# Performance work log

Measured on AMD Instinct MI355X. Metric: run time of the kernel, lower is better.

The kernel has to match this reference:

```python
import jax, jax.numpy as jnp
import numpy as np

ALPHA, BETA, LAMB, GAMMA = 1.0, 1.0, 1e-4, 1.0
K_NN, TAU = 50, 0.1
EPS = 1e-8


def _sqdist(A, B):
    # ||a - b||^2, clamped at 0 like the torch code
    d2 = (A * A).sum(1)[:, None] + (B * B).sum(1)[None, :] - 2.0 * (A @ B.T)
    return jnp.maximum(d2, 0.0)


def _mmd(s, t):
    comb = jnp.concatenate([s, t], axis=0)
    sigma_sq = jax.lax.stop_gradient(jnp.median(_sqdist(comb, comb))) / 2.0
    sigma_sq = jnp.where(sigma_sq < 1e-6, jnp.float32(1.0), sigma_sq)
    g = 1.0 / (sigma_sq + EPS)
    kxx = jnp.exp(-g * _sqdist(s, s)).mean()
    kyy = jnp.exp(-g * _sqdist(t, t)).mean()
    kxy = jnp.exp(-g * _sqdist(s, t)).mean()
    return jnp.maximum(kxx + kyy - 2.0 * kxy, 0.0)


def setup_inputs() -> dict:
    key = jax.random.key(0)
    ks = jax.random.split(key, 8)
    B, d, N, Nq, K = 256, 128, 200000, 10000, K_NN
    q_batch = jax.random.normal(ks[0], (B, d), jnp.float32)
    X = jax.random.normal(ks[1], (N, d), jnp.float32)
    W = jax.random.normal(ks[2], (d, d), jnp.float32) * (1.0 / np.sqrt(d))
    b = jnp.zeros((d,), jnp.float32)
    pre_weights = jax.random.uniform(ks[3], (Nq, K), jnp.float32)
    pre_weights = pre_weights / pre_weights.sum(1, keepdims=True)
    pre_indices = jax.random.randint(ks[4], (Nq, K), 0, N)
    q_indices = jax.random.randint(ks[5], (B,), 0, Nq)
    idx = jax.random.randint(ks[6], (B,), 0, N)
    return {"q_batch": q_batch, "X": X, "W": W, "b": b,
            "pre_weights": pre_weights, "pre_indices": pre_indices,
            "q_indices": q_indices, "idx": idx}


def reference(q_batch, X, W, b, pre_weights, pre_indices, q_indices, idx):
    Tq = q_batch @ W.T + b                                   # model(q_batch), Linear(d, d)
    # ---- MMD between mapped queries and a random database batch ----
    loss_dist = _mmd(Tq, X[idx])
    # ---- exact KNN (faiss IndexFlatL2 equivalent) on detached embeddings ----
    d2_all = _sqdist(jax.lax.stop_gradient(Tq), X)           # [B, N]
    _, post_idx = jax.lax.top_k(-d2_all, K_NN)               # [B, K] nearest neighbors
    Xn = X[post_idx]                                         # [B, K, d]
    l2 = ((Tq[:, None, :] - Xn) ** 2).sum(-1)                # [B, K] (grad flows here)
    post_w = jax.nn.softmax(-l2 / TAU, axis=1)
    # ---- union-KL, vectorized over batch (exact torch.unique semantics) ----
    pre_i = pre_indices[q_indices]                           # [B, K]
    pre_w = pre_weights[q_indices]                           # [B, K]
    cat = jnp.concatenate([pre_i, post_idx], axis=1)         # [B, 2K]
    # multiplicity of each id within the concatenated list -> collapse duplicates
    mult = (cat[:, :, None] == cat[:, None, :]).sum(-1).astype(jnp.float32)  # [B, 2K]
    p_raw = jnp.einsum('bmk,bk->bm',
                       (cat[:, :, None] == pre_i[:, None, :]).astype(jnp.float32), pre_w)
    q_raw = jnp.einsum('bmk,bk->bm',
                       (cat[:, :, None] == post_idx[:, None, :]).astype(jnp.float32), post_w)
    p_c = jnp.maximum(p_raw, EPS)
    q_c = jnp.maximum(q_raw, EPS)
    p = p_c / (p_c / mult).sum(1, keepdims=True)             # normalize over union
    q = q_c / (q_c / mult).sum(1, keepdims=True)
    kl = ((p * (jnp.log(p) - jnp.log(q))) / mult).sum(1)     # KL(p || q) per sample
    loss_knn = kl.mean()
    # ---- L2 regularization of model params & anchor loss ----
    loss_reg = 0.5 * ((W ** 2).sum() + (b ** 2).sum())
    loss_anchor = ((Tq - q_batch) ** 2).sum(1).mean()
    total = ALPHA * loss_dist + BETA * loss_knn + LAMB * loss_reg + GAMMA * loss_anchor
    return jnp.stack([total, loss_dist, loss_knn, loss_anchor])
```

## Files before the change

kernel.cpp:

```cpp
#include <hip/hip_runtime.h>
#include <cstdint>

#define D 128
#define NPTS 200000
#define KNN 50
#define CAP 8192
#define NS 8192
#define SLACK 2.0f
#define EB 2048

#define OFF_ACC    0
#define OFF_SEL    256
#define OFF_CNT    1024
#define OFF_HIST0  17408
#define OFF_HIST12 148480
#define ZERO_BYTES 214016
#define OFF_COMB   214016
#define OFF_D2     476160
#define OFF_XN     1524736
#define OFF_SAMP   2324736
#define OFF_EBUF   2324736
#define OFF_THR    10713344
#define OFF_CANDI  10714368
#define OFF_BCNT   19102976
#define OFF_TQSW   27491584
#define OFF_XBF    27557120
#define OFF_ANCP   78757120
#define OFF_WREGP  78758144

typedef __attribute__((ext_vector_type(8))) short bf16x8;
typedef __attribute__((ext_vector_type(4))) float f32x4;
typedef const __attribute__((address_space(1))) void* gas_p;
typedef __attribute__((address_space(3))) void* las_p;

__device__ __forceinline__ unsigned fkey(float f) {
    unsigned u = __float_as_uint(f);
    return u ^ ((unsigned)((int)u >> 31) | 0x80000000u);
}

__device__ __forceinline__ void stage8k(const unsigned short* __restrict__ g,
                                        unsigned short* l, int w, int lane)
{
    #pragma unroll
    for (int j = 0; j < 2; j++) {
        const unsigned short* gp = g + j * 2048 + w * 512 + lane * 8;
        unsigned short* lp = l + j * 2048 + w * 512;
        __builtin_amdgcn_global_load_lds((gas_p)gp, (las_p)lp, 16, 0, 0);
    }
}

__global__ void k_phase1(const float* __restrict__ q, const float* __restrict__ X,
                         const float* __restrict__ W, const float* __restrict__ bb,
                         const int* __restrict__ idx, float* __restrict__ comb,
                         unsigned short* __restrict__ tqsw, unsigned short* __restrict__ xbf,
                         float* __restrict__ xn, float* __restrict__ ancp,
                         float* __restrict__ wregp, float* __restrict__ wszero)
{
    const int blk = blockIdx.x, t = threadIdx.x;
    if (blk < 12500) {
        __shared__ float xr4[4][16];
        const int lr = t & 15;
        const float4* src = (const float4*)(X + ((long)(blk * 16 + lr)) * D + (t >> 4) * 8);
        float4 v0 = src[0], v1 = src[1];
        uint4 pk;
        pk.x = (__float_as_uint(v0.x) >> 16) | (__float_as_uint(v0.y) & 0xFFFF0000u);
        pk.y = (__float_as_uint(v0.z) >> 16) | (__float_as_uint(v0.w) & 0xFFFF0000u);
        pk.z = (__float_as_uint(v1.x) >> 16) | (__float_as_uint(v1.y) & 0xFFFF0000u);
        pk.w = (__float_as_uint(v1.z) >> 16) | (__float_as_uint(v1.w) & 0xFFFF0000u);
        *(uint4*)(xbf + (long)blk * 2048 + t * 8) = pk;
        float ssq = v0.x*v0.x + v0.y*v0.y + v0.z*v0.z + v0.w*v0.w
                  + v1.x*v1.x + v1.y*v1.y + v1.z*v1.z + v1.w*v1.w;
        ssq += __shfl_down(ssq, 32);
        ssq += __shfl_down(ssq, 16);
        if ((t & 63) < 16) xr4[t >> 6][lr] = ssq;
        __syncthreads();
        if (t < 16) xn[blk * 16 + t] = xr4[0][t] + xr4[1][t] + xr4[2][t] + xr4[3][t];
    } else if (blk < 12628) {
        __shared__ float rowv[2][D];
        __shared__ float red[2][D];
        const int half = t >> 7, tt = t & 127;
        const int row = (blk - 12500) * 2 + half;
        rowv[half][tt] = q[row * D + tt];
        __syncthreads();
        float s = 0.f;
        const float* wr = W + tt * D;
        #pragma unroll 4
        for (int k = 0; k < D; k++) s = fmaf(rowv[half][k], wr[k], s);
        s += bb[tt];
        comb[row * D + tt] = s;
        unsigned ub = __float_as_uint(s);
        unsigned short hv = (unsigned short)((ub + 0x7fffu + ((ub >> 16) & 1u)) >> 16);
        int ksb = tt >> 5, quad = (tt & 31) >> 3, jj = tt & 7;
        int lane = quad * 16 + (row & 15);
        tqsw[(row >> 4) * 2048 + ksb * 512 + lane * 8 + jj] = hv;
        float dd = s - rowv[half][tt];
        red[half][tt] = dd * dd;
        __syncthreads();
        for (int off = 64; off > 0; off >>= 1) { if (tt < off) red[half][tt] += red[half][tt + off]; __syncthreads(); }
        if (tt == 0) ancp[row] = red[half][0];
    } else if (blk < 12756) {
        const int half = t >> 7, tt = t & 127;
        const int i = (blk - 12628) * 2 + half;
        comb[(256 + i) * D + tt] = X[(long)idx[i] * D + tt];
    } else if (blk < 12760) {
        __shared__ float wred[4];
        const int base = (blk - 12756) * 4096;
        float s = 0.f;
        #pragma unroll 4
        for (int k = 0; k < 16; k++) { float v = W[base + k * 256 + t]; s = fmaf(v, v, s); }
        if (blk == 12756 && t < D) { float v = bb[t]; s = fmaf(v, v, s); }
        #pragma unroll
        for (int off = 32; off > 0; off >>= 1) s += __shfl_down(s, off);
        if ((t & 63) == 0) wred[t >> 6] = s;
        __syncthreads();
        if (t == 0) wregp[blk - 12756] = wred[0] + wred[1] + wred[2] + wred[3];
    } else {
        uint4* z = (uint4*)wszero;
        const uint4 zz = make_uint4(0u, 0u, 0u, 0u);
        for (int i = (blk - 12760) * 256 + t; i < (ZERO_BYTES / 16); i += 1024) z[i] = zz;
    }
}

__global__ void k_d2m(const float* __restrict__ comb, float* __restrict__ D2w,
                      unsigned* __restrict__ hist0, const unsigned short* __restrict__ tqsw,
                      const unsigned short* __restrict__ xbf, const float* __restrict__ xn,
                      float* __restrict__ samp)
{
    __shared__ __align__(16) char smraw[51456];
    const int b = blockIdx.x, t = threadIdx.x;
    if (b < 1024) {
        float (*cj)[D + 1] = (float(*)[D + 1])smraw;
        float (*ci)[D]     = (float(*)[D])(smraw + 33024);
        unsigned* h        = (unsigned*)(smraw + 35072);
        const int ib = b >> 3, jb = b & 7;
        const int w = t >> 6, l = t & 63;
        for (int m = t; m < 4096; m += 256) h[m] = 0;
        const int irow = ib * 4 + w;
        ci[w][l] = comb[irow * D + l];
        ci[w][l + 64] = comb[irow * D + l + 64];
        const float4* src = (const float4*)(comb + (jb * 64) * D);
        #pragma unroll
        for (int m = 0; m < 8; m++) {
            int u = m * 256 + t;
            int r = u >> 5, c = u & 31;
            float4 v = src[u];
            cj[r][c * 4 + 0] = v.x; cj[r][c * 4 + 1] = v.y; cj[r][c * 4 + 2] = v.z; cj[r][c * 4 + 3] = v.w;
        }
        __syncthreads();
        float s = 0.f;
        #pragma unroll 4
        for (int k = 0; k < D; k++) { float d = ci[w][k] - cj[l][k]; s = fmaf(d, d, s); }
        D2w[irow * 512 + jb * 64 + l] = s;
        atomicAdd(&h[__float_as_uint(s) >> 20], 1u);
        __syncthreads();
        const int sh = (ib + jb) & 7;
        for (int m = t; m < 4096; m += 256) { unsigned v = h[m]; if (v) atomicAdd(&hist0[m * 8 + sh], v); }
    } else {
        unsigned short* sb = (unsigned short*)smraw;
        const int w = t >> 6, lane = t & 63;
        const int lr = lane & 15, quad = lane >> 4;
        const int ck = b - 1024;
        stage8k(xbf + (long)ck * 4096, sb, w, lane);
        bf16x8 a[4][4];
        #pragma unroll
        for (int i = 0; i < 4; i++)
            #pragma unroll
            for (int ks = 0; ks < 4; ks++)
                a[i][ks] = *(const bf16x8*)(tqsw + (w * 4 + i) * 2048 + ks * 512 + lane * 8);
        __syncthreads();
        #pragma unroll
        for (int tt = 0; tt < 2; tt++) {
            const int r = (ck * 2 + tt) * 16 + lr;
            float xnv = xn[r];
            bf16x8 bfr[4];
            #pragma unroll
            for (int ks = 0; ks < 4; ks++)
                bfr[ks] = *(const bf16x8*)(sb + tt * 2048 + ks * 512 + lane * 8);
            f32x4 acc4[4];
            #pragma unroll
            for (int i = 0; i < 4; i++) acc4[i] = (f32x4){0.f, 0.f, 0.f, 0.f};
            #pragma unroll
            for (int ks = 0; ks < 4; ks++)
                #pragma unroll
                for (int i = 0; i < 4; i++)
                    acc4[i] = __builtin_amdgcn_mfma_f32_16x16x32_bf16(a[i][ks], bfr[ks], acc4[i], 0, 0, 0);
            #pragma unroll
            for (int i = 0; i < 4; i++)
                #pragma unroll
                for (int reg = 0; reg < 4; reg++) {
                    int qq = w * 64 + i * 16 + quad * 4 + reg;
                    samp[qq * NS + r] = xnv - 2.f * acc4[i][reg];
                }
        }
    }
}

__global__ void k_h1thr(const float* __restrict__ D2w, unsigned* __restrict__ hist12,
                        const unsigned* __restrict__ hist0, unsigned* __restrict__ sel,
                        const float* __restrict__ samp, float* __restrict__ thr)
{
    __shared__ unsigned buf[8192];
    __shared__ unsigned bins[4096];
    __shared__ unsigned part[256];
    __shared__ unsigned selll[4];
    __shared__ unsigned wred[4];
    const int t = threadIdx.x;
    if (blockIdx.x < 256) {
        unsigned s = 0;
        #pragma unroll
        for (int m = 0; m < 16; m++) {
            int bin = t * 16 + m;
            unsigned bs = 0;
            #pragma unroll
            for (int sh = 0; sh < 8; sh++) bs += hist0[bin * 8 + sh];
            bins[bin] = bs;
            s += bs;
        }
        part[t] = s;
        for (int m = t; m < 8192; m += 256) buf[m] = 0;
        __syncthreads();
        if (t == 0) {
            for (int tg = 0; tg < 2; tg++) {
                unsigned r = tg ? 131072u : 131071u;
                int c = 0;
                while (part[c] <= r) { r -= part[c]; c++; }
                int b = c * 16;
                while (bins[b] <= r) { r -= bins[b]; b++; }
                selll[2 * tg] = (unsigned)b; selll[2 * tg + 1] = r;
            }
            if (blockIdx.x == 0) {
                sel[0] = selll[0]; sel[1] = selll[1]; sel[2] = selll[2]; sel[3] = selll[3];
            }
        }
        __syncthreads();
        unsigned p0 = selll[0], p1 = selll[2];
        const int e0 = blockIdx.x * 1024;
        for (int m = 0; m < 4; m++) {
            unsigned key = __float_as_uint(D2w[e0 + m * 256 + t]);
            if ((key >> 20) == p0) atomicAdd(&buf[(key >> 8) & 0xFFFu], 1u);
            if ((key >> 20) == p1) atomicAdd(&buf[4096 + ((key >> 8) & 0xFFFu)], 1u);
        }
        __syncthreads();
        for (int m = t; m < 8192; m += 256) { unsigned v = buf[m]; if (v) atomicAdd(&hist12[m], v); }
    } else {
        const int q = blockIdx.x - 256;
        unsigned kreg[32];
        #pragma unroll
        for (int i = 0; i < 32; i++) kreg[i] = fkey(samp[q * NS + i * 256 + t]);
        unsigned v = 0;
        for (int bit = 31; bit >= 0; bit--) {
            unsigned trial = v | (1u << bit);
            unsigned c = 0;
            #pragma unroll
            for (int i = 0; i < 32; i++) c += (kreg[i] < trial) ? 1u : 0u;
            #pragma unroll
            for (int off = 32; off > 0; off >>= 1) c += __shfl_down(c, off);
            if ((t & 63) == 0) wred[t >> 6] = c;
            __syncthreads();
            unsigned total = wred[0] + wred[1] + wred[2] + wred[3];
            __syncthreads();
            if (total <= (unsigned)(KNN - 1)) v = trial;
        }
        if (t == 0) {
            unsigned orig = (v & 0x80000000u) ? (v ^ 0x80000000u) : ~v;
            thr[q] = __uint_as_float(orig) + SLACK;
        }
    }
}

#define FILT_BODY(SBUF)                                                              \
    do {                                                                             \
        _Pragma("unroll")                                                            \
        for (int tt = 0; tt < 2; tt++) {                                             \
            const int r = (ck * 2 + tt) * 16 + lr;                                   \
            float xnv = xn[r];                                                       \
            bf16x8 bv[4];                                                            \
            _Pragma("unroll")                                                        \
            for (int ks2 = 0; ks2 < 4; ks2++)                                        \
                bv[ks2] = *(const bf16x8*)(SBUF + tt * 2048 + ks2 * 512 + lane * 8); \
            f32x4 acc4[4];                                                           \
            _Pragma("unroll")                                                        \
            for (int i = 0; i < 4; i++) acc4[i] = (f32x4){0.f, 0.f, 0.f, 0.f};       \
            _Pragma("unroll")                                                        \
            for (int ks2 = 0; ks2 < 4; ks2++)                                        \
                _Pragma("unroll")                                                    \
                for (int i = 0; i < 4; i++)                                          \
                    acc4[i] = __builtin_amdgcn_mfma_f32_16x16x32_bf16(a[i][ks2], bv[ks2], acc4[i], 0, 0, 0); \
            _Pragma("unroll")                                                        \
            for (int i = 0; i < 4; i++)                                              \
                _Pragma("unroll")                                                    \
                for (int reg = 0; reg < 4; reg++) {                                  \
                    float s = xnv - 2.f * acc4[i][reg];                              \
                    if (s <= th_r[i][reg]) {                                         \
                        unsigned qq = (unsigned)(w * 64 + i * 16 + quad * 4 + reg);  \
                        unsigned p = atomicAdd(&lcnt, 1u);                           \
                        if (p < 1024u) lbuf[p] = (qq << 18) | (unsigned)r;           \
                        else {                                                       \
                            unsigned dd2 = gbase + p;                                \
                            if (dd2 < EB) eb[dd2] = (qq << 18) | (unsigned)r;        \
                        }                                                            \
                    }                                                                \
                }                                                                    \
        }                                                                            \
    } while (0)

__global__ __launch_bounds__(256) void k_filt2(const unsigned short* __restrict__ tqsw,
    const unsigned short* __restrict__ xbf, const float* __restrict__ xn,
    const float* __restrict__ thr, unsigned* __restrict__ ebuf, unsigned* __restrict__ bcnt,
    const float* __restrict__ D2w, unsigned* __restrict__ hist12,
    unsigned* __restrict__ sel)
{
    if (blockIdx.x >= 1024) {
        __shared__ unsigned h2c[512];
        __shared__ unsigned part2[256];
        __shared__ unsigned pfx[2];
        __shared__ unsigned rr[2];
        const int t = threadIdx.x;
        for (int tg = 0; tg < 2; tg++) {
            const unsigned* hh = hist12 + tg * 4096;
            unsigned s = 0;
            for (int m = 0; m < 16; m++) s += hh[t * 16 + m];
            part2[t] = s;
            __syncthreads();
            if (t == 0) {
                unsigned r = sel[1 + 2 * tg];
                int c = 0;
                while (part2[c] <= r) { r -= part2[c]; c++; }
                int b = c * 16;
                while (hh[b] <= r) { r -= hh[b]; b++; }
                pfx[tg] = (sel[2 * tg] << 12) | (unsigned)b;
                rr[tg] = r;
            }
            __syncthreads();
        }
        if (blockIdx.x == 1024 && t == 0) {
            sel[4] = pfx[0]; sel[5] = rr[0]; sel[6] = pfx[1]; sel[7] = rr[1];
        }
        h2c[t] = 0; h2c[256 + t] = 0;
        __syncthreads();
        unsigned p0 = pfx[0], p1 = pfx[1];
        const int e0 = (blockIdx.x - 1024) * 1024;
        for (int m = 0; m < 4; m++) {
            unsigned key = __float_as_uint(D2w[e0 + m * 256 + t]);
            if ((key >> 8) == p0) atomicAdd(&h2c[key & 0xFFu], 1u);
            if ((key >> 8) == p1) atomicAdd(&h2c[256 + (key & 0xFFu)], 1u);
        }
        __syncthreads();
        unsigned* gp = hist12 + 8192;
        unsigned v0 = h2c[t], v1 = h2c[256 + t];
        if (v0) atomicAdd(&gp[t], v0);
        if (v1) atomicAdd(&gp[4096 + t], v1);
        return;
    }
    __shared__ unsigned short sbA[4096];
    __shared__ unsigned short sbB[4096];
    __shared__ unsigned lbuf[1024];
    __shared__ unsigned lcnt;
    __shared__ unsigned gbase;
    const int t = threadIdx.x;
    const int w = t >> 6, lane = t & 63;
    const int lr = lane & 15, quad = lane >> 4;
    unsigned* eb = ebuf + (unsigned)blockIdx.x * EB;
    bf16x8 a[4][4];
    #pragma unroll
    for (int i = 0; i < 4; i++)
        #pragma unroll
        for (int ks = 0; ks < 4; ks++)
            a[i][ks] = *(const bf16x8*)(tqsw + (w * 4 + i) * 2048 + ks * 512 + lane * 8);
    float th_r[4][4];
    #pragma unroll
    for (int i = 0; i < 4; i++)
        #pragma unroll
        for (int reg = 0; reg < 4; reg++)
            th_r[i][reg] = thr[w * 64 + i * 16 + quad * 4 + reg];
    int ck = blockIdx.x;
    bool phaseA = true;
    if (t == 0) { lcnt = 0; gbase = 0; }
    stage8k(xbf + (long)ck * 4096, sbA, w, lane);
    __syncthreads();
    while (true) {
        const int ckn = ck + 1024;
        const bool has = ckn < 6250;
        if (phaseA) {
            if (has) stage8k(xbf + (long)ckn * 4096, sbB, w, lane);
            FILT_BODY(sbA);
        } else {
            if (has) stage8k(xbf + (long)ckn * 4096, sbA, w, lane);
            FILT_BODY(sbB);
        }
        __syncthreads();
        unsigned n = lcnt;
        if (!has || n >= 512u) {
            unsigned nf = (n < 1024u) ? n : 1024u;
            unsigned gb = gbase;
            for (unsigned m = t; m < nf; m += 256) {
                unsigned d = gb + m;
                if (d < EB) eb[d] = lbuf[m];
            }
            __syncthreads();
            if (t == 0) { gbase = gb + n; lcnt = 0; }
            __syncthreads();
        }
        if (!has) break;
        ck = ckn; phaseA = !phaseA;
    }
    if (t == 0) bcnt[blockIdx.x] = (gbase < EB) ? gbase : EB;
}

__global__ __launch_bounds__(256) void k_scatmmd(const unsigned* __restrict__ ebuf,
    const unsigned* __restrict__ bcnt, int* __restrict__ cand_i, unsigned* __restrict__ cnt,
    const float* __restrict__ D2w, const unsigned* __restrict__ hist12,
    const unsigned* __restrict__ sel, float* __restrict__ acc)
{
    const int t = threadIdx.x;
    if (blockIdx.x >= 128) {
        __shared__ unsigned h2[512];
        __shared__ float gsh;
        __shared__ float part[12];
        const int w = t >> 6;
        h2[t] = hist12[8192 + t];
        h2[256 + t] = hist12[8192 + 4096 + t];
        __syncthreads();
        if (t == 0) {
            unsigned key[2];
            for (int tg = 0; tg < 2; tg++) {
                unsigned r = sel[5 + 2 * tg];
                const unsigned* hh = h2 + tg * 256;
                int b = 0;
                while (hh[b] <= r) { r -= hh[b]; b++; }
                key[tg] = (sel[4 + 2 * tg] << 8) | (unsigned)b;
            }
            float med = 0.5f * (__uint_as_float(key[0]) + __uint_as_float(key[1]));
            float ssq = 0.5f * med;
            if (ssq < 1e-6f) ssq = 1.0f;
            gsh = 1.0f / (ssq + 1e-8f);
        }
        __syncthreads();
        const float g = gsh;
        float s[3] = {0.f, 0.f, 0.f};
        const int e0 = (blockIdx.x - 128) * 1024;
        #pragma unroll
        for (int m = 0; m < 4; m++) {
            int e = e0 + m * 256 + t;
            int i = e >> 9, j = e & 511;
            float v = expf(-g * D2w[e]);
            int qd = (i < 256) ? ((j < 256) ? 0 : 2) : ((j < 256) ? 2 : 1);
            s[qd] += v;
        }
        #pragma unroll
        for (int c = 0; c < 3; c++) {
            float x = s[c];
            #pragma unroll
            for (int off = 32; off > 0; off >>= 1) x += __shfl_down(x, off);
            if ((t & 63) == 0) part[w * 3 + c] = x;
        }
        __syncthreads();
        if (t == 0)
            for (int c = 0; c < 3; c++)
                atomicAdd(&acc[2 + c], part[c] + part[3 + c] + part[6 + c] + part[9 + c]);
        return;
    }
    __shared__ unsigned hist[256];
    __shared__ unsigned startp[256];
    const int b0 = blockIdx.x * 8;
    hist[t] = 0;
    __syncthreads();
    for (int b = b0; b < b0 + 8; b++) {
        unsigned n = bcnt[b];
        const unsigned* e = ebuf + (unsigned)b * EB;
        for (unsigned m = t; m < n; m += 256)
            atomicAdd(&hist[e[m] >> 18], 1u);
    }
    __syncthreads();
    unsigned c = hist[t];
    if (c) {
        unsigned base = atomicAdd(&cnt[t * 16], c);
        startp[t] = ((unsigned)t << 13) + base;
    }
    __syncthreads();
    for (int b = b0; b < b0 + 8; b++) {
        unsigned n = bcnt[b];
        const unsigned* e = ebuf + (unsigned)b * EB;
        for (unsigned m = t; m < n; m += 256) {
            unsigned ent = e[m];
            unsigned qq = ent >> 18;
            unsigned pos = atomicAdd(&startp[qq], 1u);
            if (pos < ((qq + 1u) << 13)) cand_i[pos] = (int)(ent & 0x3FFFFu);
        }
    }
}

__global__ __launch_bounds__(1024) void k_rp(const float* __restrict__ comb,
                        const float* __restrict__ X,
                        const int* __restrict__ cand_i, const unsigned* __restrict__ cnt,
                        const int* __restrict__ pri,
                        const float* __restrict__ prw, const int* __restrict__ qix,
                        const float* __restrict__ xn,
                        float* __restrict__ acc, unsigned* __restrict__ sel,
                        const float* __restrict__ ancp, const float* __restrict__ wregp,
                        float* __restrict__ out)
{
    __shared__ unsigned ks[CAP];
    __shared__ float qrow[D];
    __shared__ unsigned wred[16];
    __shared__ unsigned wpos, eqn;
    __shared__ int eq[64];
    __shared__ int pidx[KNN];
    __shared__ float l2s[KNN];
    __shared__ float pw[KNN];
    __shared__ int ci[100];
    __shared__ float pwv[50], qwv[50];
    __shared__ float pterm[100], qterm[100], kterm[100];
    __shared__ float Sp, Sq;
    const int q = blockIdx.x, t = threadIdx.x;
    if (t < D) qrow[t] = comb[q * D + t];
    if (t == 0) { wpos = 0; eqn = 0; }
    unsigned nn = cnt[q * 16];
    const int n = (nn < (unsigned)CAP) ? (int)nn : CAP;
    __syncthreads();
    const int g = t >> 3, j = t & 7;
    for (int m = g; m < n; m += 128) {
        int r = cand_i[q * CAP + m];
        const float4* xr = (const float4*)(X + (long)r * D);
        float s = 0.f;
        #pragma unroll
        for (int p = 0; p < 4; p++) {
            float4 xv = xr[j * 4 + p];
            float4 qv = *(const float4*)&qrow[(j * 4 + p) * 4];
            s = fmaf(xv.x, qv.x, fmaf(xv.y, qv.y, fmaf(xv.z, qv.z, fmaf(xv.w, qv.w, s))));
        }
        s += __shfl_down(s, 4); s += __shfl_down(s, 2); s += __shfl_down(s, 1);
        if (j == 0) ks[m] = fkey(xn[r] - 2.f * s);
    }
    __syncthreads();
    unsigned kreg[8];
    #pragma unroll
    for (int i = 0; i < 8; i++) {
        int m = i * 1024 + t;
        kreg[i] = (m < n) ? ks[m] : 0xFFFFFFFFu;
    }
    int kk = KNN - 1; if (kk > n - 1) kk = n - 1;
    unsigned v = 0;
    for (int bit = 31; bit >= 0; bit--) {
        unsigned trial = v | (1u << bit);
        unsigned c = 0;
        #pragma unroll
        for (int i = 0; i < 8; i++) c += (kreg[i] < trial) ? 1u : 0u;
        #pragma unroll
        for (int off = 32; off > 0; off >>= 1) c += __shfl_down(c, off);
        if ((t & 63) == 0) wred[t >> 6] = c;
        __syncthreads();
        unsigned total = 0;
        #pragma unroll
        for (int i = 0; i < 16; i++) total += wred[i];
        __syncthreads();
        if (total <= (unsigned)kk) v = trial;
    }
    for (int m = t; m < n; m += 1024) {
        if (ks[m] < v) {
            unsigned p = atomicAdd(&wpos, 1u);
            pidx[p] = cand_i[q * CAP + m];
        } else if (ks[m] == v) {
            unsigned p = atomicAdd(&eqn, 1u);
            if (p < 64) eq[p] = cand_i[q * CAP + m];
        }
    }
    __syncthreads();
    if (t == 0) {
        int c1 = (int)wpos, need = KNN - c1;
        int ne = (eqn < 64u) ? (int)eqn : 64;
        for (int a = 0; a < ne; a++)
            for (int b2 = a + 1; b2 < ne; b2++)
                if (eq[b2] < eq[a]) { int tmp = eq[a]; eq[a] = eq[b2]; eq[b2] = tmp; }
        for (int a = 0; a < need && a < ne; a++) pidx[c1 + a] = eq[a];
    }
    __syncthreads();
    for (int nb = g; nb < KNN; nb += 128) {
        long r = pidx[nb];
        const float4* xr = (const float4*)(X + r * D);
        float s = 0.f;
        #pragma unroll
        for (int p = 0; p < 4; p++) {
            float4 xv = xr[j * 4 + p];
            float4 qv = *(const float4*)&qrow[(j * 4 + p) * 4];
            float d0 = qv.x - xv.x, d1 = qv.y - xv.y, d2 = qv.z - xv.z, d3 = qv.w - xv.w;
            s += d0 * d0 + d1 * d1 + d2 * d2 + d3 * d3;
        }
        s += __shfl_down(s, 4); s += __shfl_down(s, 2); s += __shfl_down(s, 1);
        if (j == 0) l2s[nb] = s;
    }
    int qi = qix[q];
    if (t >= 128 && t < 178) { int k = t - 128; ci[k] = pri[qi * 50 + k]; pwv[k] = prw[qi * 50 + k]; }
    __syncthreads();
    if (t < 64) {
        float logit = (t < KNN) ? (-l2s[t] * 10.0f) : -3.4e38f;
        float m = logit;
        #pragma unroll
        for (int off = 32; off > 0; off >>= 1) m = fmaxf(m, __shfl_down(m, off));
        m = __shfl(m, 0);
        float e = (t < KNN) ? expf(logit - m) : 0.f;
        float ss = e;
        #pragma unroll
        for (int off = 32; off > 0; off >>= 1) ss += __shfl_down(ss, off);
        ss = __shfl(ss, 0);
        if (t < KNN) pw[t] = e / ss;
    }
    __syncthreads();
    if (t < 50) { ci[50 + t] = pidx[t]; qwv[t] = pw[t]; }
    __syncthreads();
    float pc = 0.f, qc = 0.f, mult = 0.f;
    if (t < 100) {
        int c = ci[t];
        float pr = 0.f, qr = 0.f;
        for (int k = 0; k < 50; k++) {
            bool m1 = (c == ci[k]); bool m2 = (c == ci[50 + k]);
            mult += (m1 ? 1.f : 0.f) + (m2 ? 1.f : 0.f);
            pr += m1 ? pwv[k] : 0.f;
            qr += m2 ? qwv[k] : 0.f;
        }
        pc = fmaxf(pr, 1e-8f); qc = fmaxf(qr, 1e-8f);
        pterm[t] = pc / mult; qterm[t] = qc / mult;
    }
    __syncthreads();
    if (t == 0) { float a = 0.f, b2 = 0.f; for (int m = 0; m < 100; m++) { a += pterm[m]; b2 += qterm[m]; } Sp = a; Sq = b2; }
    __syncthreads();
    if (t < 100) {
        float p = pc / Sp, qq2 = qc / Sq;
        kterm[t] = (p * (logf(p) - logf(qq2))) / mult;
    }
    __syncthreads();
    if (t == 0) {
        float s = 0.f;
        for (int m = 0; m < 100; m++) s += kterm[m];
        atomicAdd(&acc[1], s);
        __threadfence();
        unsigned old = atomicAdd(&sel[15], 1u);
        if (old == 255u) {
            __threadfence();
            float lknn = atomicAdd(&acc[1], 0.f) / 256.f;
            float reg = 0.f;
            #pragma unroll
            for (int m = 0; m < 4; m++) reg += wregp[m];
            reg *= 0.5f;
            float anc = 0.f;
            for (int m = 0; m < 256; m++) anc += ancp[m];
            float lanc = anc / 256.f;
            float kxx = acc[2] / 65536.f, kyy = acc[3] / 65536.f, kxy = acc[4] / 131072.f;
            float ld = fmaxf(kxx + kyy - 2.f * kxy, 0.f);
            out[0] = ld + lknn + 1e-4f * reg + lanc;
            out[1] = ld; out[2] = lknn; out[3] = lanc;
        }
    }
}

extern "C" void kernel_launch(void* const* d_in, const int* in_sizes, int n_in,
                              void* d_out, int out_size, void* d_ws, size_t ws_size,
                              hipStream_t stream)
{
    (void)in_sizes; (void)n_in; (void)out_size; (void)ws_size;
    const float* q   = (const float*)d_in[0];
    const float* X   = (const float*)d_in[1];
    const float* W   = (const float*)d_in[2];
    const float* bb  = (const float*)d_in[3];
    const float* prw = (const float*)d_in[4];
    const int*   pri = (const int*)d_in[5];
    const int*   qix = (const int*)d_in[6];
    const int*   idx = (const int*)d_in[7];
    float* out = (float*)d_out;
    char* ws = (char*)d_ws;
    float*    acc   = (float*)(ws + OFF_ACC);
    unsigned* sel   = (unsigned*)(ws + OFF_SEL);
    unsigned* cnt   = (unsigned*)(ws + OFF_CNT);
    unsigned* hist0 = (unsigned*)(ws + OFF_HIST0);
    unsigned* hist12= (unsigned*)(ws + OFF_HIST12);
    float*    comb  = (float*)(ws + OFF_COMB);
    float*    D2w   = (float*)(ws + OFF_D2);
    float*    xn    = (float*)(ws + OFF_XN);
    float*    samp  = (float*)(ws + OFF_SAMP);
    float*    thr   = (float*)(ws + OFF_THR);
    int*      cix   = (int*)(ws + OFF_CANDI);
    unsigned* ebuf  = (unsigned*)(ws + OFF_EBUF);
    unsigned* bcnt  = (unsigned*)(ws + OFF_BCNT);
    unsigned short* tqsw = (unsigned short*)(ws + OFF_TQSW);
    unsigned short* xbf  = (unsigned short*)(ws + OFF_XBF);
    float*    ancp  = (float*)(ws + OFF_ANCP);
    float*    wregp = (float*)(ws + OFF_WREGP);

    hipLaunchKernelGGL(k_phase1,  dim3(12764),   dim3(256), 0, stream, q, X, W, bb, idx, comb, tqsw, xbf, xn, ancp, wregp, acc);
    hipLaunchKernelGGL(k_d2m,     dim3(1280),    dim3(256), 0, stream, comb, D2w, hist0, tqsw, xbf, xn, samp);
    hipLaunchKernelGGL(k_h1thr,   dim3(512),     dim3(256), 0, stream, D2w, hist12, hist0, sel, samp, thr);
    hipLaunchKernelGGL(k_filt2,   dim3(1280),    dim3(256), 0, stream, tqsw, xbf, xn, thr, ebuf, bcnt, D2w, hist12, sel);
    hipLaunchKernelGGL(k_scatmmd, dim3(384),     dim3(256), 0, stream, ebuf, bcnt, cix, cnt, D2w, hist12, sel, acc);
    hipLaunchKernelGGL(k_rp,      dim3(256),     dim3(1024), 0, stream, comb, X, cix, cnt, pri, prw, qix, xn, acc, sel, ancp, wregp, out);
}
```

Measured before the change: 358.9 us.

## Carry bf16 filter scores through scatter to prune exact fp32 rescoring in k_rp

The bf16 MFMA filter now stores each candidate's approximate distance key alongside its index, and the scatter kernel propagates these keys into a per-query array. k_rp first runs a radix select on the approximate keys, keeps only candidates within a fixed band of the approximate 50th distance, and recomputes exact fp32 distances just for that subset. This cuts the per-query gathers of X rows and dot products in the final kernel. In exchange it adds extra global writes of scores, a second select pass, and correctness relies on the band being wide enough to cover bf16 error; it falls back to the full path if more than 2048 candidates survive.

After: 360.2 us. No clear change (+0.4%).

```diff
diff --git a/kernel.cpp b/kernel.cpp
--- a/kernel.cpp
+++ b/kernel.cpp
@@ -7,6 +7,7 @@
 #define CAP 8192
 #define NS 8192
 #define SLACK 2.0f
+#define BAND 4.0f
 #define EB 2048
 
 #define OFF_ACC    0
@@ -22,11 +23,13 @@
 #define OFF_EBUF   2324736
 #define OFF_THR    10713344
 #define OFF_CANDI  10714368
-#define OFF_BCNT   19102976
+#define OFF_SCO    19102976
 #define OFF_TQSW   27491584
 #define OFF_XBF    27557120
 #define OFF_ANCP   78757120
 #define OFF_WREGP  78758144
+#define OFF_BCNT   78758400
+#define OFF_KSA    78774272
 
 typedef __attribute__((ext_vector_type(8))) short bf16x8;
 typedef __attribute__((ext_vector_type(4))) float f32x4;
@@ -294,10 +297,10 @@
                     if (s <= th_r[i][reg]) {                                         \
                         unsigned qq = (unsigned)(w * 64 + i * 16 + quad * 4 + reg);  \
                         unsigned p = atomicAdd(&lcnt, 1u);                           \
-                        if (p < 1024u) lbuf[p] = (qq << 18) | (unsigned)r;           \
+                        if (p < 1024u) { lbuf[p] = (qq << 18) | (unsigned)r; lsco[p] = fkey(s); } \
                         else {                                                       \
                             unsigned dd2 = gbase + p;                                \
-                            if (dd2 < EB) eb[dd2] = (qq << 18) | (unsigned)r;        \
+                            if (dd2 < EB) { eb[dd2] = (qq << 18) | (unsigned)r; ebs[dd2] = fkey(s); } \
                         }                                                            \
                     }                                                                \
                 }                                                                    \
@@ -306,9 +309,9 @@
 
 __global__ __launch_bounds__(256) void k_filt2(const unsigned short* __restrict__ tqsw,
     const unsigned short* __restrict__ xbf, const float* __restrict__ xn,
-    const float* __restrict__ thr, unsigned* __restrict__ ebuf, unsigned* __restrict__ bcnt,
-    const float* __restrict__ D2w, unsigned* __restrict__ hist12,
-    unsigned* __restrict__ sel)
+    const float* __restrict__ thr, unsigned* __restrict__ ebuf, unsigned* __restrict__ esco,
+    unsigned* __restrict__ bcnt, const float* __restrict__ D2w,
+    unsigned* __restrict__ hist12, unsigned* __restrict__ sel)
 {
     if (blockIdx.x >= 1024) {
         __shared__ unsigned h2c[512];
@@ -355,12 +358,14 @@
     __shared__ unsigned short sbA[4096];
     __shared__ unsigned short sbB[4096];
     __shared__ unsigned lbuf[1024];
+    __shared__ unsigned lsco[1024];
     __shared__ unsigned lcnt;
     __shared__ unsigned gbase;
     const int t = threadIdx.x;
     const int w = t >> 6, lane = t & 63;
     const int lr = lane & 15, quad = lane >> 4;
-    unsigned* eb = ebuf + (unsigned)blockIdx.x * EB;
+    unsigned* eb  = ebuf + (unsigned)blockIdx.x * EB;
+    unsigned* ebs = esco + (unsigned)blockIdx.x * EB;
     bf16x8 a[4][4];
     #pragma unroll
     for (int i = 0; i < 4; i++)
@@ -395,7 +400,7 @@
             unsigned gb = gbase;
             for (unsigned m = t; m < nf; m += 256) {
                 unsigned d = gb + m;
-                if (d < EB) eb[d] = lbuf[m];
+                if (d < EB) { eb[d] = lbuf[m]; ebs[d] = lsco[m]; }
             }
             __syncthreads();
             if (t == 0) { gbase = gb + n; lcnt = 0; }
@@ -408,7 +413,8 @@
 }
 
 __global__ __launch_bounds__(256) void k_scatmmd(const unsigned* __restrict__ ebuf,
-    const unsigned* __restrict__ bcnt, int* __restrict__ cand_i, unsigned* __restrict__ cnt,
+    const unsigned* __restrict__ esco, const unsigned* __restrict__ bcnt,
+    int* __restrict__ cand_i, unsigned* __restrict__ ksa, unsigned* __restrict__ cnt,
     const float* __restrict__ D2w, const unsigned* __restrict__ hist12,
     const unsigned* __restrict__ sel, float* __restrict__ acc)
 {
@@ -481,18 +487,21 @@
     for (int b = b0; b < b0 + 8; b++) {
         unsigned n = bcnt[b];
         const unsigned* e = ebuf + (unsigned)b * EB;
+        const unsigned* e2 = esco + (unsigned)b * EB;
         for (unsigned m = t; m < n; m += 256) {
             unsigned ent = e[m];
+            unsigned sk = e2[m];
             unsigned qq = ent >> 18;
             unsigned pos = atomicAdd(&startp[qq], 1u);
-            if (pos < ((qq + 1u) << 13)) cand_i[pos] = (int)(ent & 0x3FFFFu);
+            if (pos < ((qq + 1u) << 13)) { cand_i[pos] = (int)(ent & 0x3FFFFu); ksa[pos] = sk; }
         }
     }
 }
 
 __global__ __launch_bounds__(1024) void k_rp(const float* __restrict__ comb,
                         const float* __restrict__ X,
-                        const int* __restrict__ cand_i, const unsigned* __restrict__ cnt,
+                        const int* __restrict__ cand_i, const unsigned* __restrict__ ksa,
+                        const unsigned* __restrict__ cnt,
                         const int* __restrict__ pri,
                         const float* __restrict__ prw, const int* __restrict__ qix,
                         const float* __restrict__ xn,
@@ -501,9 +510,11 @@
                         float* __restrict__ out)
 {
     __shared__ unsigned ks[CAP];
+    __shared__ int sidx[2048];
+    __shared__ unsigned eks[2048];
     __shared__ float qrow[D];
     __shared__ unsigned wred[16];
-    __shared__ unsigned wpos, eqn;
+    __shared__ unsigned scnt, wpos, eqn;
     __shared__ int eq[64];
     __shared__ int pidx[KNN];
     __shared__ float l2s[KNN];
@@ -514,38 +525,85 @@
     __shared__ float Sp, Sq;
     const int q = blockIdx.x, t = threadIdx.x;
     if (t < D) qrow[t] = comb[q * D + t];
-    if (t == 0) { wpos = 0; eqn = 0; }
+    if (t == 0) { wpos = 0; eqn = 0; scnt = 0; }
     unsigned nn = cnt[q * 16];
     const int n = (nn < (unsigned)CAP) ? (int)nn : CAP;
-    __syncthreads();
-    const int g = t >> 3, j = t & 7;
-    for (int m = g; m < n; m += 128) {
-        int r = cand_i[q * CAP + m];
-        const float4* xr = (const float4*)(X + (long)r * D);
-        float s = 0.f;
-        #pragma unroll
-        for (int p = 0; p < 4; p++) {
-            float4 xv = xr[j * 4 + p];
-            float4 qv = *(const float4*)&qrow[(j * 4 + p) * 4];
-            s = fmaf(xv.x, qv.x, fmaf(xv.y, qv.y, fmaf(xv.z, qv.z, fmaf(xv.w, qv.w, s))));
-        }
-        s += __shfl_down(s, 4); s += __shfl_down(s, 2); s += __shfl_down(s, 1);
-        if (j == 0) ks[m] = fkey(xn[r] - 2.f * s);
-    }
-    __syncthreads();
-    unsigned kreg[8];
+    for (int m = t; m < n; m += 1024) ks[m] = ksa[q * CAP + m];
+    __syncthreads();
+    unsigned kregA[8];
     #pragma unroll
     for (int i = 0; i < 8; i++) {
         int m = i * 1024 + t;
-        kreg[i] = (m < n) ? ks[m] : 0xFFFFFFFFu;
+        kregA[i] = (m < n) ? ks[m] : 0xFFFFFFFFu;
     }
     int kk = KNN - 1; if (kk > n - 1) kk = n - 1;
+    unsigned va = 0;
+    for (int bit = 31; bit >= 0; bit--) {
+        unsigned trial = va | (1u << bit);
+        unsigned c = 0;
+        #pragma unroll
+        for (int i = 0; i < 8; i++) c += (kregA[i] < trial) ? 1u : 0u;
+        #pragma unroll
+        for (int off = 32; off > 0; off >>= 1) c += __shfl_down(c, off);
+        if ((t & 63) == 0) wred[t >> 6] = c;
+        __syncthreads();
+        unsigned total = 0;
+        #pragma unroll
+        for (int i = 0; i < 16; i++) total += wred[i];
+        __syncthreads();
+        if (total <= (unsigned)kk) va = trial;
+    }
+    unsigned ovaf = (va & 0x80000000u) ? (va ^ 0x80000000u) : ~va;
+    unsigned vkeep = fkey(__uint_as_float(ovaf) + BAND);
+    for (int m = t; m < n; m += 1024) {
+        if (ks[m] <= vkeep) {
+            unsigned p = atomicAdd(&scnt, 1u);
+            if (p < 2048u) sidx[p] = cand_i[q * CAP + m];
+        }
+    }
+    __syncthreads();
+    const bool cpath = (scnt <= 2048u);
+    const int ns = cpath ? (int)scnt : n;
+    const int g = t >> 3, j = t & 7;
+    if (cpath) {
+        for (int m = g; m < ns; m += 128) {
+            int r = sidx[m];
+            const float4* xr = (const float4*)(X + (long)r * D);
+            float s = 0.f;
+            #pragma unroll
+            for (int p = 0; p < 4; p++) {
+                float4 xv = xr[j * 4 + p];
+                float4 qv = *(const float4*)&qrow[(j * 4 + p) * 4];
+                s = fmaf(xv.x, qv.x, fmaf(xv.y, qv.y, fmaf(xv.z, qv.z, fmaf(xv.w, qv.w, s))));
+            }
+            s += __shfl_down(s, 4); s += __shfl_down(s, 2); s += __shfl_down(s, 1);
+            if (j == 0) eks[m] = fkey(xn[r] - 2.f * s);
+        }
+    } else {
+        for (int m = g; m < ns; m += 128) {
+            int r = cand_i[q * CAP + m];
+            const float4* xr = (const float4*)(X + (long)r * D);
+            float s = 0.f;
+            #pragma unroll
+            for (int p = 0; p < 4; p++) {
+                float4 xv = xr[j * 4 + p];
+                float4 qv = *(const float4*)&qrow[(j * 4 + p) * 4];
+                s = fmaf(xv.x, qv.x, fmaf(xv.y, qv.y, fmaf(xv.z, qv.z, fmaf(xv.w, qv.w, s))));
+            }
+            s += __shfl_down(s, 4); s += __shfl_down(s, 2); s += __shfl_down(s, 1);
+            if (j == 0) ks[m] = fkey(xn[r] - 2.f * s);
+        }
+    }
+    __syncthreads();
+    kk = KNN - 1; if (kk > ns - 1) kk = ns - 1;
     unsigned v = 0;
     for (int bit = 31; bit >= 0; bit--) {
         unsigned trial = v | (1u << bit);
         unsigned c = 0;
-        #pragma unroll
-        for (int i = 0; i < 8; i++) c += (kreg[i] < trial) ? 1u : 0u;
+        for (int m = t; m < ns; m += 1024) {
+            unsigned kv = cpath ? eks[m] : ks[m];
+            c += (kv < trial) ? 1u : 0u;
+        }
         #pragma unroll
         for (int off = 32; off > 0; off >>= 1) c += __shfl_down(c, off);
         if ((t & 63) == 0) wred[t >> 6] = c;
@@ -556,13 +614,15 @@
         __syncthreads();
         if (total <= (unsigned)kk) v = trial;
     }
-    for (int m = t; m < n; m += 1024) {
-        if (ks[m] < v) {
+    for (int m = t; m < ns; m += 1024) {
+        unsigned kv = cpath ? eks[m] : ks[m];
+        int r = cpath ? sidx[m] : cand_i[q * CAP + m];
+        if (kv < v) {
             unsigned p = atomicAdd(&wpos, 1u);
-            pidx[p] = cand_i[q * CAP + m];
-        } else if (ks[m] == v) {
+            pidx[p] = r;
+        } else if (kv == v) {
             unsigned p = atomicAdd(&eqn, 1u);
-            if (p < 64) eq[p] = cand_i[q * CAP + m];
+            if (p < 64) eq[p] = r;
         }
     }
     __syncthreads();
@@ -680,7 +740,9 @@
     float*    thr   = (float*)(ws + OFF_THR);
     int*      cix   = (int*)(ws + OFF_CANDI);
     unsigned* ebuf  = (unsigned*)(ws + OFF_EBUF);
+    unsigned* esco  = (unsigned*)(ws + OFF_SCO);
     unsigned* bcnt  = (unsigned*)(ws + OFF_BCNT);
+    unsigned* ksa   = (unsigned*)(ws + OFF_KSA);
     unsigned short* tqsw = (unsigned short*)(ws + OFF_TQSW);
     unsigned short* xbf  = (unsigned short*)(ws + OFF_XBF);
     float*    ancp  = (float*)(ws + OFF_ANCP);
@@ -689,7 +751,7 @@
     hipLaunchKernelGGL(k_phase1,  dim3(12764),   dim3(256), 0, stream, q, X, W, bb, idx, comb, tqsw, xbf, xn, ancp, wregp, acc);
     hipLaunchKernelGGL(k_d2m,     dim3(1280),    dim3(256), 0, stream, comb, D2w, hist0, tqsw, xbf, xn, samp);
     hipLaunchKernelGGL(k_h1thr,   dim3(512),     dim3(256), 0, stream, D2w, hist12, hist0, sel, samp, thr);
-    hipLaunchKernelGGL(k_filt2,   dim3(1280),    dim3(256), 0, stream, tqsw, xbf, xn, thr, ebuf, bcnt, D2w, hist12, sel);
-    hipLaunchKernelGGL(k_scatmmd, dim3(384),     dim3(256), 0, stream, ebuf, bcnt, cix, cnt, D2w, hist12, sel, acc);
-    hipLaunchKernelGGL(k_rp,      dim3(256),     dim3(1024), 0, stream, comb, X, cix, cnt, pri, prw, qix, xn, acc, sel, ancp, wregp, out);
-}
+    hipLaunchKernelGGL(k_filt2,   dim3(1280),    dim3(256), 0, stream, tqsw, xbf, xn, thr, ebuf, esco, bcnt, D2w, hist12, sel);
+    hipLaunchKernelGGL(k_scatmmd, dim3(384),     dim3(256), 0, stream, ebuf, esco, bcnt, cix, ksa, cnt, D2w, hist12, sel, acc);
+    hipLaunchKernelGGL(k_rp,      dim3(256),     dim3(1024), 0, stream, comb, X, cix, ksa, cnt, pri, prw, qix, xn, acc, sel, ancp, wregp, out);
+}
```
